# Kernel optimization log

Measured on AMD Instinct MI355X. Metric: run time of the kernel, lower is better.

The kernel has to match this reference:

```python
import jax, jax.numpy as jnp
import numpy as np

B, S, H, D, BS = 4, 1024, 32, 128, 16  # batch, seq, heads, head_dim, block_size
E = H * D  # 4096 hidden
NB = S // BS  # blocks per sequence


def _rope(x, cos, sin):
    # x: [T, H, D]; cos/sin: [T, D//2]  (GPT-NeoX half-split rotary)
    d2 = x.shape[-1] // 2
    x1, x2 = x[..., :d2], x[..., d2:]
    c, s = cos[:, None, :], sin[:, None, :]
    return jnp.concatenate([x1 * c - x2 * s, x2 * c + x1 * s], axis=-1)


def setup_inputs() -> dict:
    key = jax.random.key(0)
    ks = jax.random.split(key, 6)
    hidden_states = jax.random.normal(ks[0], (B * S, E), jnp.float32)
    qkv_weight = jax.random.normal(ks[1], (3, E, E), jnp.float32) * 0.02
    o_weight = jax.random.normal(ks[2], (E, E), jnp.float32) * 0.02
    # rotary tables per token position (sequences are contiguous, equal length)
    inv_freq = 1.0 / (10000.0 ** (jnp.arange(0, D, 2, dtype=jnp.float32) / D))
    pos = jnp.tile(jnp.arange(S, dtype=jnp.float32), B)  # [T]
    ang = pos[:, None] * inv_freq[None, :]  # [T, D//2]
    cos, sin = jnp.cos(ang), jnp.sin(ang)
    k_cache = jnp.zeros((B * NB, H, BS, D), jnp.float32)
    v_cache = jnp.zeros((B * NB, H, BS, D), jnp.float32)
    block_tables = jnp.arange(B * NB, dtype=jnp.int32).reshape(B, NB)
    cu_seqlens = (jnp.arange(B + 1, dtype=jnp.int32) * S)
    sequence_lengths = jnp.full((B,), S, dtype=jnp.int32)
    return {"hidden_states": hidden_states, "qkv_weight": qkv_weight, "o_weight": o_weight,
            "cos": cos, "sin": sin, "k_cache": k_cache, "v_cache": v_cache,
            "block_tables": block_tables, "cu_seqlens": cu_seqlens,
            "sequence_lengths": sequence_lengths}


def reference(hidden_states, qkv_weight, o_weight, cos, sin, k_cache, v_cache,
              block_tables, cu_seqlens, sequence_lengths):
    T = hidden_states.shape[0]
    # fused QKV projection: bmm of [3,T,E] x [3,E,E]
    qkv = jnp.einsum('te,kef->ktf', hidden_states, qkv_weight).reshape(3, T, H, D)
    q, k, v = qkv[0], qkv[1], qkv[2]
    # rotary embedding on q, k
    q = _rope(q, cos, sin)
    k = _rope(k, cos, sin)
    # paged KV-cache memcpy: write k/v into [num_blocks, H, BS, D] via block_tables
    k_blk = k.reshape(B, NB, BS, H, D).transpose(0, 1, 3, 2, 4).reshape(B * NB, H, BS, D)
    v_blk = v.reshape(B, NB, BS, H, D).transpose(0, 1, 3, 2, 4).reshape(B * NB, H, BS, D)
    bt = block_tables.reshape(-1)
    k_cache = k_cache.at[bt].set(k_blk)
    v_cache = v_cache.at[bt].set(v_blk)
    # varlen causal attention (equal-length sequences -> batched causal attention)
    qb = q.reshape(B, S, H, D)
    kb = k.reshape(B, S, H, D)
    vb = v.reshape(B, S, H, D)
    sm_scale = 1.0 / jnp.sqrt(jnp.float32(D))
    scores = jnp.einsum('bqhd,bkhd->bhqk', qb, kb) * sm_scale
    causal = jnp.tril(jnp.ones((S, S), bool))
    scores = jnp.where(causal[None, None], scores, jnp.finfo(scores.dtype).min)
    probs = jax.nn.softmax(scores, axis=-1)
    attn = jnp.einsum('bhqk,bkhd->bqhd', probs, vb).reshape(T, E)
    out = attn @ o_weight  # o_proj (bias-free linear)
    return out, k_cache, v_cache
```

## Files before the change

### kernel.cpp

```cpp
#include <hip/hip_runtime.h>

#define B_  4
#define S_  1024
#define H_  32
#define D_  128
#define E_  4096
#define T_  4096
#define NB_ 64
#define BS_ 16

typedef __attribute__((ext_vector_type(8))) __bf16 bf16x8;
typedef __attribute__((ext_vector_type(4))) __bf16 bf16x4;
typedef __attribute__((ext_vector_type(4))) float f32x4;

__device__ __forceinline__ void gload_lds16(const __bf16* g, __bf16* l) {
  __builtin_amdgcn_global_load_lds((const __attribute__((address_space(1))) void*)g,
                                   (__attribute__((address_space(3))) void*)l, 16, 0, 0);
}

__global__ __launch_bounds__(256) void k_convert_hs(const float* __restrict__ x,
                                                    __bf16* __restrict__ y, int n4) {
  int i = blockIdx.x * 256 + threadIdx.x;
  if (i < n4) {
    float4 v = ((const float4*)x)[i];
    bf16x4 o;
    o[0] = (__bf16)v.x; o[1] = (__bf16)v.y; o[2] = (__bf16)v.z; o[3] = (__bf16)v.w;
    ((bf16x4*)y)[i] = o;
  }
}

__global__ __launch_bounds__(256) void k_transpose_w(const float* __restrict__ W,
                                                     __bf16* __restrict__ WT) {
  __shared__ float tile[32][33];
  const float* Wm = W + (size_t)blockIdx.z * E_ * E_;
  __bf16* WTm = WT + (size_t)blockIdx.z * E_ * E_;
  int e0 = blockIdx.x * 32, f0 = blockIdx.y * 32;
  int tx = threadIdx.x & 31, ty = threadIdx.x >> 5;
  for (int i = ty; i < 32; i += 8) tile[i][tx] = Wm[(size_t)(e0 + i) * E_ + f0 + tx];
  __syncthreads();
  for (int i = ty; i < 32; i += 8) WTm[(size_t)(f0 + i) * E_ + e0 + tx] = (__bf16)tile[tx][i];
}

__global__ __launch_bounds__(256) void k_transpose_v(const __bf16* __restrict__ v,
                                                     __bf16* __restrict__ vT) {
  __shared__ __bf16 tile[32][33];
  size_t bh = blockIdx.z;
  const __bf16* vp = v + bh * S_ * D_;
  __bf16* vtp = vT + bh * S_ * D_;
  int s0 = blockIdx.x * 32, d0 = blockIdx.y * 32;
  int tx = threadIdx.x & 31, ty = threadIdx.x >> 5;
  for (int i = ty; i < 32; i += 8) tile[i][tx] = vp[(size_t)(s0 + i) * D_ + d0 + tx];
  __syncthreads();
  for (int i = ty; i < 32; i += 8) vtp[(size_t)(d0 + i) * S_ + s0 + tx] = tile[tx][i];
}

__global__ __launch_bounds__(256) void k_rope(__bf16* __restrict__ q, __bf16* __restrict__ k,
                                              const __bf16* __restrict__ v,
                                              const float* __restrict__ cosb,
                                              const float* __restrict__ sinb,
                                              const int* __restrict__ bt,
                                              float* __restrict__ kc, float* __restrict__ vc) {
  int idx = blockIdx.x * 256 + threadIdx.x;
  int j = idx & 63;
  int s = (idx >> 6) & (S_ - 1);
  int h = (idx >> 16) & (H_ - 1);
  int b = idx >> 21;
  size_t base = (((size_t)b * H_ + h) * S_ + s) * D_;
  float c  = cosb[(size_t)(b * S_ + s) * 64 + j];
  float sn = sinb[(size_t)(b * S_ + s) * 64 + j];
  float q1 = (float)q[base + j], q2 = (float)q[base + j + 64];
  float k1 = (float)k[base + j], k2 = (float)k[base + j + 64];
  float q1n = q1 * c - q2 * sn, q2n = q2 * c + q1 * sn;
  float k1n = k1 * c - k2 * sn, k2n = k2 * c + k1 * sn;
  q[base + j] = (__bf16)q1n; q[base + j + 64] = (__bf16)q2n;
  k[base + j] = (__bf16)k1n; k[base + j + 64] = (__bf16)k2n;
  int nb = s >> 4, sb = s & 15;
  int blk = bt[b * NB_ + nb];
  size_t cidx = (((size_t)blk * H_ + h) * BS_ + sb) * D_;
  kc[cidx + j] = k1n; kc[cidx + j + 64] = k2n;
  vc[cidx + j] = (float)v[base + j];
  vc[cidx + j + 64] = (float)v[base + j + 64];
}

#define GEMM_BODY                                                                  \
  __shared__ __align__(16) __bf16 As[128 * 32];                                    \
  __shared__ __align__(16) __bf16 Bs[128 * 32];                                    \
  int tid = threadIdx.x;                                                           \
  int wid = tid >> 6, lane = tid & 63, l15 = lane & 15, quad = lane >> 4;          \
  int wy = wid >> 1, wx = wid & 1;                                                 \
  int m0 = blockIdx.x * 128, n0 = blockIdx.y * 128;                                \
       \
  int srow = wid * 32 + (lane >> 2);                                               \
  int scol = (lane & 3) * 8;                                                       \
  const __bf16* Ag = A + (size_t)(m0 + srow) * E_ + scol;                          \
  const __bf16* Bg = BT + (size_t)(n0 + srow) * E_ + scol;                         \
  __bf16* Al = As + srow * 32 + scol;                                              \
  __bf16* Bl = Bs + srow * 32 + scol;                                              \
  f32x4 acc[4][4] = {};                                                            \
  for (int k0 = 0; k0 < E_; k0 += 32) {                                            \
    gload_lds16(Ag + k0, Al);                                                      \
    gload_lds16(Ag + k0 + (size_t)16 * E_, Al + 16 * 32);                          \
    gload_lds16(Bg + k0, Bl);                                                      \
    gload_lds16(Bg + k0 + (size_t)16 * E_, Bl + 16 * 32);                          \
    __syncthreads();                                                               \
    bf16x8 af[4], bfr[4];                                                          \
    for (int i = 0; i < 4; i++) af[i]  = *(const bf16x8*)&As[(wy * 64 + i * 16 + l15) * 32 + quad * 8]; \
    for (int j = 0; j < 4; j++) bfr[j] = *(const bf16x8*)&Bs[(wx * 64 + j * 16 + l15) * 32 + quad * 8]; \
    for (int i = 0; i < 4; i++)                                                    \
      for (int j = 0; j < 4; j++)                                                  \
        acc[i][j] = __builtin_amdgcn_mfma_f32_16x16x32_bf16(af[i], bfr[j], acc[i][j], 0, 0, 0); \
    __syncthreads();                                                               \
  }

__global__ __launch_bounds__(256) void k_gemm_qkv(const __bf16* __restrict__ A,
                                                  const __bf16* __restrict__ BT,
                                                  __bf16* __restrict__ qkvb) {
  GEMM_BODY
  for (int i = 0; i < 4; i++) {
    int tbase = m0 + wy * 64 + i * 16 + quad * 4;
    for (int j = 0; j < 4; j++) {
      int n = n0 + wx * 64 + j * 16 + l15;
      int kk = n >> 12, nl = n & 4095;
      int h = nl >> 7, d = nl & 127;
      for (int r = 0; r < 4; r++) {
        int t = tbase + r;
        int bb = t >> 10, s = t & 1023;
        size_t idx = ((((size_t)kk * B_ + bb) * H_ + h) * S_ + s) * D_ + d;
        qkvb[idx] = (__bf16)acc[i][j][r];
      }
    }
  }
}

__global__ __launch_bounds__(256) void k_gemm_out(const __bf16* __restrict__ A,
                                                  const __bf16* __restrict__ BT,
                                                  float* __restrict__ out) {
  GEMM_BODY
  for (int i = 0; i < 4; i++) {
    int tbase = m0 + wy * 64 + i * 16 + quad * 4;
    for (int j = 0; j < 4; j++) {
      int n = n0 + wx * 64 + j * 16 + l15;
      for (int r = 0; r < 4; r++)
        out[(size_t)(tbase + r) * E_ + n] = acc[i][j][r];
    }
  }
}

__global__ __launch_bounds__(256) void k_attn(const __bf16* __restrict__ q,
                                              const __bf16* __restrict__ k,
                                              const __bf16* __restrict__ vT,
                                              __bf16* __restrict__ attn) {
  __shared__ __align__(16) __bf16 Qs[64][136];
  __shared__ __align__(16) __bf16 Ks[64][136];
  __shared__ __align__(16) __bf16 Vs[128][72];
  __shared__ __align__(16) __bf16 Ps[4][16][72];

  int q0 = blockIdx.x * 64;
  int h = blockIdx.y, b = blockIdx.z;
  int tid = threadIdx.x, wid = tid >> 6, lane = tid & 63, l15 = lane & 15, quad = lane >> 4;

  size_t bh = (size_t)b * H_ + h;
  const __bf16* Qp = q + bh * S_ * D_;
  const __bf16* Kp = k + bh * S_ * D_;
  const __bf16* Vp = vT + bh * (size_t)D_ * S_;

  for (int c = tid; c < 1024; c += 256) {
    int r = c >> 4, dp = (c & 15) * 8;
    *(int4*)&Qs[r][dp] = *(const int4*)&Qp[(size_t)(q0 + r) * D_ + dp];
  }
  __syncthreads();
  bf16x8 aq[4];
  for (int ks = 0; ks < 4; ks++) aq[ks] = *(const bf16x8*)&Qs[wid * 16 + l15][ks * 32 + quad * 8];

  float m_run[4], l_run[4];
  f32x4 o_acc[8] = {};
  for (int r = 0; r < 4; r++) { m_run[r] = -1e30f; l_run[r] = 0.f; }
  const float sm_scale = 0.08838834764831845f;

  int kend = q0 + 64;
  for (int sk0 = 0; sk0 < kend; sk0 += 64) {
    __syncthreads();
    for (int c = tid; c < 1024; c += 256) {
      int r = c >> 4, dp = (c & 15) * 8;
      *(int4*)&Ks[r][dp] = *(const int4*)&Kp[(size_t)(sk0 + r) * D_ + dp];
    }
    for (int c = tid; c < 1024; c += 256) {
      int d = c >> 3, sp = (c & 7) * 8;
      *(int4*)&Vs[d][sp] = *(const int4*)&Vp[(size_t)d * S_ + sk0 + sp];
    }
    __syncthreads();

    f32x4 st[4] = {};
    for (int nt = 0; nt < 4; nt++)
      for (int ks = 0; ks < 4; ks++) {
        bf16x8 bk = *(const bf16x8*)&Ks[nt * 16 + l15][ks * 32 + quad * 8];
        st[nt] = __builtin_amdgcn_mfma_f32_16x16x32_bf16(aq[ks], bk, st[nt], 0, 0, 0);
      }

    int qg = q0 + wid * 16 + quad * 4;
    float mnew[4], alpha[4];
    for (int r = 0; r < 4; r++) {
      float rmax = -1e30f;
      for (int nt = 0; nt < 4; nt++) {
        int kg = sk0 + nt * 16 + l15;
        float vsc = st[nt][r] * sm_scale;
        if (kg > qg + r) vsc = -1e30f;
        st[nt][r] = vsc;
        rmax = fmaxf(rmax, vsc);
      }
      for (int off = 1; off < 16; off <<= 1) rmax = fmaxf(rmax, __shfl_xor(rmax, off));
      mnew[r] = fmaxf(m_run[r], rmax);
      alpha[r] = __expf(m_run[r] - mnew[r]);
      float s_ = 0.f;
      for (int nt = 0; nt < 4; nt++) {
        float p = __expf(st[nt][r] - mnew[r]);
        st[nt][r] = p;
        s_ += p;
      }
      for (int off = 1; off < 16; off <<= 1) s_ += __shfl_xor(s_, off);
      l_run[r] = l_run[r] * alpha[r] + s_;
      m_run[r] = mnew[r];
    }

    for (int nt = 0; nt < 4; nt++)
      for (int r = 0; r < 4; r++)
        Ps[wid][quad * 4 + r][nt * 16 + l15] = (__bf16)st[nt][r];

    for (int dt = 0; dt < 8; dt++)
      for (int r = 0; r < 4; r++)
        o_acc[dt][r] *= alpha[r];

    __syncthreads();

    for (int ks2 = 0; ks2 < 2; ks2++) {
      bf16x8 ap = *(const bf16x8*)&Ps[wid][l15][ks2 * 32 + quad * 8];
      for (int dt = 0; dt < 8; dt++) {
        bf16x8 bv = *(const bf16x8*)&Vs[dt * 16 + l15][ks2 * 32 + quad * 8];
        o_acc[dt] = __builtin_amdgcn_mfma_f32_16x16x32_bf16(ap, bv, o_acc[dt], 0, 0, 0);
      }
    }
  }

  size_t trow = (size_t)b * S_ + q0 + wid * 16 + quad * 4;
  for (int dt = 0; dt < 8; dt++) {
    int e = h * D_ + dt * 16 + l15;
    for (int r = 0; r < 4; r++) {
      float val = o_acc[dt][r] / l_run[r];
      attn[(trow + r) * E_ + e] = (__bf16)val;
    }
  }
}

extern "C" void kernel_launch(void* const* d_in, const int* in_sizes, int n_in,
                              void* d_out, int out_size, void* d_ws, size_t ws_size,
                              hipStream_t stream) {
  const float* hs    = (const float*)d_in[0];
  const float* qkv_w = (const float*)d_in[1];
  const float* o_w   = (const float*)d_in[2];
  const float* cosb  = (const float*)d_in[3];
  const float* sinb  = (const float*)d_in[4];
  const int*   bt    = (const int*)d_in[7];

  float* out = (float*)d_out;
  float* kc  = out + (size_t)T_ * E_;
  float* vc  = kc + (size_t)B_ * NB_ * H_ * BS_ * D_;

  char* ws = (char*)d_ws;
  __bf16* hsb  = (__bf16*)ws;
  __bf16* wT   = (__bf16*)(ws + 33554432);
  __bf16* oT   = wT + (size_t)3 * E_ * E_;
  __bf16* qb   = (__bf16*)(ws + 167772160);
  __bf16* kb   = qb + (size_t)B_ * H_ * S_ * D_;
  __bf16* vb   = kb + (size_t)B_ * H_ * S_ * D_;
  __bf16* vTt  = (__bf16*)(ws + 268435456);
  __bf16* attn = hsb;

  k_convert_hs<<<dim3(T_ * E_ / 4 / 256), dim3(256), 0, stream>>>(hs, hsb, T_ * E_ / 4);
  k_transpose_w<<<dim3(128, 128, 3), dim3(256), 0, stream>>>(qkv_w, wT);
  k_transpose_w<<<dim3(128, 128, 1), dim3(256), 0, stream>>>(o_w, oT);
  k_gemm_qkv<<<dim3(32, 96), dim3(256), 0, stream>>>(hsb, wT, qb);
  k_rope<<<dim3(32768), dim3(256), 0, stream>>>(qb, kb, vb, cosb, sinb, bt, kc, vc);
  k_transpose_v<<<dim3(32, 4, 128), dim3(256), 0, stream>>>(vb, vTt);
  k_attn<<<dim3(16, 32, 4), dim3(256), 0, stream>>>(qb, kb, vTt, attn);
  k_gemm_out<<<dim3(32, 32), dim3(256), 0, stream>>>(attn, oT, out);
}
```

Baseline: 1.529 ms.

## Rewrite GEMMs with 256x256 tiles, 4-stage LDS ring pipeline and XCD swizzle

```diff
diff --git a/kernel.cpp b/kernel.cpp
--- a/kernel.cpp
+++ b/kernel.cpp
@@ -8,6 +8,7 @@
 #define T_  4096
 #define NB_ 64
 #define BS_ 16
+#define NT_ 128
 
 typedef __attribute__((ext_vector_type(8))) __bf16 bf16x8;
 typedef __attribute__((ext_vector_type(4))) __bf16 bf16x4;
@@ -82,44 +83,70 @@
   vc[cidx + j + 64] = (float)v[base + j + 64];
 }
 
-#define GEMM_BODY                                                                  \
-  __shared__ __align__(16) __bf16 As[128 * 32];                                    \
-  __shared__ __align__(16) __bf16 Bs[128 * 32];                                    \
+
+#define STAGE256(tt) {                                                             \
+    int _b = (tt) & 3;                                                             \
+    const __bf16* _ag = Ag + (size_t)(tt) * 32;                                    \
+    const __bf16* _bg = Bg + (size_t)(tt) * 32;                                    \
+    __bf16* _al = &ring[_b][0][0] + wid * 512 + lane * 8;                          \
+    __bf16* _bl = &ring[_b][1][0] + wid * 512 + lane * 8;                          \
+    gload_lds16(_ag, _al);                                                         \
+    gload_lds16(_ag + (size_t)128 * E_, _al + 4096);                               \
+    gload_lds16(_bg, _bl);                                                         \
+    gload_lds16(_bg + (size_t)128 * E_, _bl + 4096);                               \
+  }
+
+#define COMPUTE256(tt) {                                                           \
+    int _b = (tt) & 3;                                                             \
+    const __bf16* _ab = &ring[_b][0][0];                                           \
+    const __bf16* _bb = &ring[_b][1][0];                                           \
+    bf16x8 afr[8], bfr[4];                                                         \
+    _Pragma("unroll")                                                              \
+    for (int i = 0; i < 8; i++)                                                    \
+      afr[i] = *(const bf16x8*)&_ab[(wm * 128 + i * 16 + l15) * 32 + quad * 8];    \
+    _Pragma("unroll")                                                              \
+    for (int j = 0; j < 4; j++)                                                    \
+      bfr[j] = *(const bf16x8*)&_bb[(wn * 64 + j * 16 + l15) * 32 + quad * 8];     \
+    __builtin_amdgcn_s_setprio(1);                                                 \
+    _Pragma("unroll")                                                              \
+    for (int i = 0; i < 8; i++)                                                    \
+      _Pragma("unroll")                                                            \
+      for (int j = 0; j < 4; j++)                                                  \
+        acc[i][j] = __builtin_amdgcn_mfma_f32_16x16x32_bf16(afr[i], bfr[j], acc[i][j], 0, 0, 0); \
+    __builtin_amdgcn_s_setprio(0);                                                 \
+  }
+
+#define GEMM256_BODY                                                               \
+  __shared__ __align__(16) __bf16 ring[4][2][256 * 32];               \
   int tid = threadIdx.x;                                                           \
   int wid = tid >> 6, lane = tid & 63, l15 = lane & 15, quad = lane >> 4;          \
-  int wy = wid >> 1, wx = wid & 1;                                                 \
-  int m0 = blockIdx.x * 128, n0 = blockIdx.y * 128;                                \
-       \
-  int srow = wid * 32 + (lane >> 2);                                               \
-  int scol = (lane & 3) * 8;                                                       \
+  int wm = wid >> 2, wn = wid & 3;                                                 \
+                               \
+  int cpx = (int)gridDim.x >> 3;                                                   \
+  int wg = ((int)blockIdx.x & 7) * cpx + ((int)blockIdx.x >> 3);                   \
+  int m0 = (wg & 15) * 256, n0 = (wg >> 4) * 256;                                  \
+  int srow = wid * 16 + (lane >> 2), scol = (lane & 3) * 8;                        \
   const __bf16* Ag = A + (size_t)(m0 + srow) * E_ + scol;                          \
   const __bf16* Bg = BT + (size_t)(n0 + srow) * E_ + scol;                         \
-  __bf16* Al = As + srow * 32 + scol;                                              \
-  __bf16* Bl = Bs + srow * 32 + scol;                                              \
-  f32x4 acc[4][4] = {};                                                            \
-  for (int k0 = 0; k0 < E_; k0 += 32) {                                            \
-    gload_lds16(Ag + k0, Al);                                                      \
-    gload_lds16(Ag + k0 + (size_t)16 * E_, Al + 16 * 32);                          \
-    gload_lds16(Bg + k0, Bl);                                                      \
-    gload_lds16(Bg + k0 + (size_t)16 * E_, Bl + 16 * 32);                          \
-    __syncthreads();                                                               \
-    bf16x8 af[4], bfr[4];                                                          \
-    for (int i = 0; i < 4; i++) af[i]  = *(const bf16x8*)&As[(wy * 64 + i * 16 + l15) * 32 + quad * 8]; \
-    for (int j = 0; j < 4; j++) bfr[j] = *(const bf16x8*)&Bs[(wx * 64 + j * 16 + l15) * 32 + quad * 8]; \
-    for (int i = 0; i < 4; i++)                                                    \
-      for (int j = 0; j < 4; j++)                                                  \
-        acc[i][j] = __builtin_amdgcn_mfma_f32_16x16x32_bf16(af[i], bfr[j], acc[i][j], 0, 0, 0); \
-    __syncthreads();                                                               \
-  }
-
-__global__ __launch_bounds__(256) void k_gemm_qkv(const __bf16* __restrict__ A,
-                                                  const __bf16* __restrict__ BT,
-                                                  __bf16* __restrict__ qkvb) {
-  GEMM_BODY
-  for (int i = 0; i < 4; i++) {
-    int tbase = m0 + wy * 64 + i * 16 + quad * 4;
+  f32x4 acc[8][4] = {};                                                            \
+  STAGE256(0) STAGE256(1) STAGE256(2)                                              \
+  for (int t = 0; t < NT_; ++t) {                                                  \
+    if (t < NT_ - 2)       { asm volatile("s_waitcnt vmcnt(8)" ::: "memory"); }    \
+    else if (t == NT_ - 2) { asm volatile("s_waitcnt vmcnt(4)" ::: "memory"); }    \
+    else                   { asm volatile("s_waitcnt vmcnt(0)" ::: "memory"); }    \
+    __builtin_amdgcn_s_barrier();                                                  \
+    if (t + 3 < NT_) STAGE256(t + 3)                                               \
+    COMPUTE256(t)                                                                  \
+  }
+
+__global__ __launch_bounds__(512, 1) void k_gemm_qkv(const __bf16* __restrict__ A,
+                                                     const __bf16* __restrict__ BT,
+                                                     __bf16* __restrict__ qkvb) {
+  GEMM256_BODY
+  for (int i = 0; i < 8; i++) {
+    int tbase = m0 + wm * 128 + i * 16 + quad * 4;
     for (int j = 0; j < 4; j++) {
-      int n = n0 + wx * 64 + j * 16 + l15;
+      int n = n0 + wn * 64 + j * 16 + l15;
       int kk = n >> 12, nl = n & 4095;
       int h = nl >> 7, d = nl & 127;
       for (int r = 0; r < 4; r++) {
@@ -132,14 +159,14 @@
   }
 }
 
-__global__ __launch_bounds__(256) void k_gemm_out(const __bf16* __restrict__ A,
-                                                  const __bf16* __restrict__ BT,
-                                                  float* __restrict__ out) {
-  GEMM_BODY
-  for (int i = 0; i < 4; i++) {
-    int tbase = m0 + wy * 64 + i * 16 + quad * 4;
+__global__ __launch_bounds__(512, 1) void k_gemm_out(const __bf16* __restrict__ A,
+                                                     const __bf16* __restrict__ BT,
+                                                     float* __restrict__ out) {
+  GEMM256_BODY
+  for (int i = 0; i < 8; i++) {
+    int tbase = m0 + wm * 128 + i * 16 + quad * 4;
     for (int j = 0; j < 4; j++) {
-      int n = n0 + wx * 64 + j * 16 + l15;
+      int n = n0 + wn * 64 + j * 16 + l15;
       for (int r = 0; r < 4; r++)
         out[(size_t)(tbase + r) * E_ + n] = acc[i][j][r];
     }
@@ -278,9 +305,9 @@
   k_convert_hs<<<dim3(T_ * E_ / 4 / 256), dim3(256), 0, stream>>>(hs, hsb, T_ * E_ / 4);
   k_transpose_w<<<dim3(128, 128, 3), dim3(256), 0, stream>>>(qkv_w, wT);
   k_transpose_w<<<dim3(128, 128, 1), dim3(256), 0, stream>>>(o_w, oT);
-  k_gemm_qkv<<<dim3(32, 96), dim3(256), 0, stream>>>(hsb, wT, qb);
+  k_gemm_qkv<<<dim3(768), dim3(512), 0, stream>>>(hsb, wT, qb);
   k_rope<<<dim3(32768), dim3(256), 0, stream>>>(qb, kb, vb, cosb, sinb, bt, kc, vc);
   k_transpose_v<<<dim3(32, 4, 128), dim3(256), 0, stream>>>(vb, vTt);
   k_attn<<<dim3(16, 32, 4), dim3(256), 0, stream>>>(qb, kb, vTt, attn);
-  k_gemm_out<<<dim3(32, 32), dim3(256), 0, stream>>>(attn, oT, out);
-}
+  k_gemm_out<<<dim3(256), dim3(512), 0, stream>>>(attn, oT, out);
+}
```

Measured after the change: 1.358 ms. 11.2% less time.
